# Optimization experiments

Hardware: AMD Instinct MI355X
Metric: run time of the kernel (lower is better)

## Reference

```python
import math
import jax, jax.numpy as jnp
import numpy as np

D = 1024
H = 16
DK = D // H
B = 4
L = 2048


def setup_inputs() -> dict:
    key = jax.random.key(0)
    ks = jax.random.split(key, 11)
    s = 1.0 / math.sqrt(D)
    return {
        "q": jax.random.normal(ks[0], (B, L, D), jnp.float32),
        "k": jax.random.normal(ks[1], (B, L, D), jnp.float32),
        "v": jax.random.normal(ks[2], (B, L, D), jnp.float32),
        "wq_w": jax.random.normal(ks[3], (D, D), jnp.float32) * s,
        "wq_b": jnp.zeros((D,), jnp.float32),
        "wk_w": jax.random.normal(ks[4], (D, D), jnp.float32) * s,
        "wk_b": jnp.zeros((D,), jnp.float32),
        "wv_w": jax.random.normal(ks[5], (D, D), jnp.float32) * s,
        "wv_b": jnp.zeros((D,), jnp.float32),
        "wo_w": jax.random.normal(ks[6], (D, D), jnp.float32) * s,
        "wo_b": jnp.zeros((D,), jnp.float32),
    }


def reference(q, k, v, wq_w, wq_b, wk_w, wk_b, wv_w, wv_b, wo_w, wo_b):
    # torch Linear: x @ W.T + b
    Q = (q @ wq_w.T + wq_b).reshape(B, L, H, DK).transpose(0, 2, 1, 3)  # [B,H,L,DK]
    K = (k @ wk_w.T + wk_b).reshape(B, -1, H, DK).transpose(0, 2, 1, 3)
    V = (v @ wv_w.T + wv_b).reshape(B, -1, H, DK).transpose(0, 2, 1, 3)
    sc = jnp.einsum("bhqd,bhkd->bhqk", Q, K) / math.sqrt(DK)  # [B,H,L,L]
    # causal mask: strictly upper triangular filled with -1e9
    cm = jnp.triu(jnp.ones((L, L), dtype=bool), 1)
    sc = jnp.where(cm, jnp.float32(-1e9), sc)
    at = jax.nn.softmax(sc, axis=-1)  # dropout p=0 (eval)
    out = jnp.einsum("bhqk,bhkd->bhqd", at, V)  # [B,H,L,DK]
    out = out.transpose(0, 2, 1, 3).reshape(B, L, D)
    return out @ wo_w.T + wo_b
```

## Files before the change

### kernel.cpp

```cpp
#include <hip/hip_runtime.h>
#include <stdint.h>

#define DD 1024
#define NH 16
#define DHEAD 64
#define NB 4
#define SEQ 2048
#define MR (NB*SEQ)
#define NT (SEQ/128)

typedef __attribute__((ext_vector_type(8))) short s8v;
typedef __attribute__((ext_vector_type(4))) float f4v;

__device__ __forceinline__ unsigned short f2bf(float f) {
  union { float f; uint32_t u; } c; c.f = f;
  uint32_t u = c.u;
  u += 0x7fffu + ((u >> 16) & 1u);
  return (unsigned short)(u >> 16);
}
__device__ __forceinline__ unsigned short f2bf_trunc(float f) {
  union { float f; uint32_t u; } c; c.f = f;
  return (unsigned short)(c.u >> 16);
}

__device__ __forceinline__ void load_lds16(const void* g, void* lds) {
  __builtin_amdgcn_global_load_lds(
      (__attribute__((address_space(1))) void*)(uintptr_t)g,
      (__attribute__((address_space(3))) void*)(uint32_t)(uintptr_t)lds,
      16, 0, 0);
}

__global__ void cvt_all(
    const float* __restrict__ q, const float* __restrict__ k, const float* __restrict__ v,
    const float* __restrict__ w0, const float* __restrict__ w1,
    const float* __restrict__ w2, const float* __restrict__ w3,
    unsigned short* __restrict__ qb, unsigned short* __restrict__ kb,
    unsigned short* __restrict__ vb,
    unsigned short* __restrict__ w0b, unsigned short* __restrict__ w1b,
    unsigned short* __restrict__ w2b, unsigned short* __restrict__ w3b)
{
  int blk = blockIdx.x;
  const float* src; unsigned short* dst; size_t off;
  if (blk < 12288) {
    int a = blk >> 12;
    src = a == 0 ? q : (a == 1 ? k : v);
    dst = a == 0 ? qb : (a == 1 ? kb : vb);
    off = (size_t)(blk & 4095) * 2048;
  } else {
    int wb = blk - 12288;
    int a = wb >> 9;
    src = a == 0 ? w0 : (a == 1 ? w1 : (a == 2 ? w2 : w3));
    dst = a == 0 ? w0b : (a == 1 ? w1b : (a == 2 ? w2b : w3b));
    off = (size_t)(wb & 511) * 2048;
  }
  size_t i = off + (size_t)threadIdx.x * 8;
  float4 a4 = *(const float4*)(src + i);
  float4 b4 = *(const float4*)(src + i + 4);
  union { unsigned short us[8]; uint4 u; } t;
  t.us[0] = f2bf(a4.x); t.us[1] = f2bf(a4.y); t.us[2] = f2bf(a4.z); t.us[3] = f2bf(a4.w);
  t.us[4] = f2bf(b4.x); t.us[5] = f2bf(b4.y); t.us[6] = f2bf(b4.z); t.us[7] = f2bf(b4.w);
  *(uint4*)(dst + i) = t.u;
}

__global__ __launch_bounds__(256, 2) void gemm_bt(
    const unsigned short* __restrict__ A,
    const unsigned short* __restrict__ Bw,
    const float* __restrict__ bias,
    float* __restrict__ Cout)
{
  __shared__ __align__(16) short As[64 * 64];
  __shared__ __align__(16) short Bs[128 * 64];
  const int linear = blockIdx.y * 8 + blockIdx.x;
  const int nx = linear >> 7;
  const int my = linear & 127;
  const int tid = threadIdx.x;
  const int wave = tid >> 6, lane = tid & 63;
  const int wm = (wave >> 1) * 32, wn = (wave & 1) * 64;
  const int lr = lane & 15, lg = lane >> 4;
  const unsigned short* Ab = A + (size_t)my * 64 * DD;
  const unsigned short* Bb = Bw + (size_t)nx * 128 * DD;

  f4v z = {0.f, 0.f, 0.f, 0.f};
  f4v acc[2][4];
  for (int mi = 0; mi < 2; mi++) for (int ni = 0; ni < 4; ni++) acc[mi][ni] = z;

  for (int k0 = 0; k0 < DD; k0 += 64) {
    __syncthreads();
    for (int i = 0; i < 2; i++) {
      int c = tid + i * 256;
      int row = c >> 3, kc = (c & 7) << 3;
      load_lds16(Ab + (size_t)row * DD + k0 + kc, As + c * 8);
    }
    for (int i = 0; i < 4; i++) {
      int c = tid + i * 256;
      int row = c >> 3, kc = (c & 7) << 3;
      load_lds16(Bb + (size_t)row * DD + k0 + kc, Bs + c * 8);
    }
    __syncthreads();
    for (int kk = 0; kk < 64; kk += 32) {
      s8v af[2], bf[4];
      for (int i = 0; i < 2; i++)
        af[i] = *(const s8v*)(As + (wm + i * 16 + lr) * 64 + kk + lg * 8);
      for (int i = 0; i < 4; i++)
        bf[i] = *(const s8v*)(Bs + (wn + i * 16 + lr) * 64 + kk + lg * 8);
      for (int mi = 0; mi < 2; mi++)
        for (int ni = 0; ni < 4; ni++)
          acc[mi][ni] = __builtin_amdgcn_mfma_f32_16x16x32_bf16(af[mi], bf[ni], acc[mi][ni], 0, 0, 0);
    }
  }
  for (int ni = 0; ni < 4; ni++) {
    int col = nx * 128 + wn + ni * 16 + lr;
    float bv = bias[col];
    for (int mi = 0; mi < 2; mi++) {
      int row0 = my * 64 + wm + mi * 16 + lg * 4;
      for (int r = 0; r < 4; r++)
        Cout[(size_t)(row0 + r) * DD + col] = acc[mi][ni][r] + bv;
    }
  }
}

__global__ __launch_bounds__(256, 2) void gemm_qkv(
    const unsigned short* __restrict__ qA, const unsigned short* __restrict__ kA,
    const unsigned short* __restrict__ vA,
    const unsigned short* __restrict__ wq, const unsigned short* __restrict__ wk,
    const unsigned short* __restrict__ wv,
    const float* __restrict__ bq, const float* __restrict__ bk, const float* __restrict__ bv,
    unsigned short* __restrict__ Qp, unsigned short* __restrict__ Kp,
    unsigned short* __restrict__ VpT)
{
  __shared__ __align__(16) short As[128 * 64];
  __shared__ __align__(16) short Bs[128 * 64];
  const int linear = blockIdx.y * 24 + blockIdx.x;
  const int nx  = linear / 192;
  const int rem = linear % 192;
  const int seg = rem >> 6;
  const int my  = rem & 63;
  const unsigned short* A  = seg == 0 ? qA : (seg == 1 ? kA : vA);
  const unsigned short* Bw = seg == 0 ? wq : (seg == 1 ? wk : wv);
  const float* bias        = seg == 0 ? bq : (seg == 1 ? bk : bv);

  const int tid = threadIdx.x;
  const int wave = tid >> 6, lane = tid & 63;
  const int wm = (wave >> 1) * 64, wn = (wave & 1) * 64;
  const int lr = lane & 15, lg = lane >> 4;
  const unsigned short* Ab = A + (size_t)my * 128 * DD;
  const unsigned short* Bb = Bw + (size_t)nx * 128 * DD;

  f4v z = {0.f, 0.f, 0.f, 0.f};
  f4v acc[4][4];
  for (int mi = 0; mi < 4; mi++) for (int ni = 0; ni < 4; ni++) acc[mi][ni] = z;

  for (int k0 = 0; k0 < DD; k0 += 64) {
    __syncthreads();
    for (int i = 0; i < 4; i++) {
      int c = tid + i * 256;
      int row = c >> 3, kc = (c & 7) << 3;
      load_lds16(Ab + (size_t)row * DD + k0 + kc, As + c * 8);
      load_lds16(Bb + (size_t)row * DD + k0 + kc, Bs + c * 8);
    }
    __syncthreads();
    for (int kk = 0; kk < 64; kk += 32) {
      s8v af[4], bf[4];
      for (int i = 0; i < 4; i++)
        af[i] = *(const s8v*)(As + (wm + i * 16 + lr) * 64 + kk + lg * 8);
      for (int i = 0; i < 4; i++)
        bf[i] = *(const s8v*)(Bs + (wn + i * 16 + lr) * 64 + kk + lg * 8);
      for (int mi = 0; mi < 4; mi++)
        for (int ni = 0; ni < 4; ni++)
          acc[mi][ni] = __builtin_amdgcn_mfma_f32_16x16x32_bf16(af[mi], bf[ni], acc[mi][ni], 0, 0, 0);
    }
  }
  if (seg < 2) {
    unsigned short* Cout = seg == 0 ? Qp : Kp;
    for (int ni = 0; ni < 4; ni++) {
      int col = nx * 128 + wn + ni * 16 + lr;
      float bv = bias[col];
      for (int mi = 0; mi < 4; mi++) {
        int row0 = my * 128 + wm + mi * 16 + lg * 4;
        for (int r = 0; r < 4; r++)
          Cout[(size_t)(row0 + r) * DD + col] = f2bf(acc[mi][ni][r] + bv);
      }
    }
  } else {
    for (int ni = 0; ni < 4; ni++) {
      int col = nx * 128 + wn + ni * 16 + lr;
      float bv = bias[col];
      int hh = col >> 6, dd = col & 63;
      for (int mi = 0; mi < 4; mi++) {
        int row0 = my * 128 + wm + mi * 16 + lg * 4;
        int bb = row0 >> 11, ll = row0 & 2047;
        uint64_t w = 0;
        for (int r = 0; r < 4; r++)
          w |= (uint64_t)f2bf(acc[mi][ni][r] + bv) << (16 * r);
        *(uint64_t*)(VpT + ((size_t)(bb * NH + hh) * 64 + dd) * SEQ + ll) = w;
      }
    }
  }
}

#define KS_STRIDE 72
#define VT_STRIDE 136
#define PS_STRIDE 72

__device__ __forceinline__ void attn_step(
    const s8v (&qf)[2][2], const s8v (&kf)[2][4],
    f4v (&o)[2][4], float (&ls)[2][4],
    int qbase, int colbase,
    const short* __restrict__ Vt, int vsub, short* __restrict__ Pw,
    int lr, int lg)
{
  const float csc = 0.125f * 1.44269504089f;
  const float FM = 14.0f;
  f4v zv = {0.f, 0.f, 0.f, 0.f};
  f4v s[2][4];
  for (int mi = 0; mi < 2; mi++) for (int ni = 0; ni < 4; ni++) s[mi][ni] = zv;
  for (int ks = 0; ks < 2; ks++)
    for (int mi = 0; mi < 2; mi++)
      for (int ni = 0; ni < 4; ni++)
        s[mi][ni] = __builtin_amdgcn_mfma_f32_16x16x32_bf16(qf[mi][ks], kf[ks][ni], s[mi][ni], 0, 0, 0);
  const bool diag = (colbase + 63 > qbase);
  for (int mi = 0; mi < 2; mi++)
    for (int ni = 0; ni < 4; ni++)
      for (int r = 0; r < 4; r++) {
        float e = __builtin_amdgcn_exp2f(fmaf(s[mi][ni][r], csc, -FM));
        if (diag) {
          int row = qbase + mi * 16 + lg * 4 + r;
          int col = colbase + ni * 16 + lr;
          e = (col > row) ? 0.f : e;
        }
        ls[mi][r] += e;
        Pw[(mi * 16 + lg * 4 + r) * PS_STRIDE + ni * 16 + lr] = (short)f2bf_trunc(e);
      }
  for (int kc2 = 0; kc2 < 2; kc2++) {
    s8v pf[2], vf[4];
    for (int mi = 0; mi < 2; mi++)
      pf[mi] = *(const s8v*)(Pw + (mi * 16 + lr) * PS_STRIDE + kc2 * 32 + lg * 8);
    for (int ni = 0; ni < 4; ni++)
      vf[ni] = *(const s8v*)(Vt + (ni * 16 + lr) * VT_STRIDE + vsub + kc2 * 32 + lg * 8);
    for (int mi = 0; mi < 2; mi++)
      for (int ni = 0; ni < 4; ni++)
        o[mi][ni] = __builtin_amdgcn_mfma_f32_16x16x32_bf16(pf[mi], vf[ni], o[mi][ni], 0, 0, 0);
  }
}

__global__ __launch_bounds__(256, 2) void fattn(
    const unsigned short* __restrict__ Qp,
    const unsigned short* __restrict__ Kp,
    const unsigned short* __restrict__ VpT,
    unsigned short* __restrict__ Op)
{
  __shared__ __align__(16) short Ks[128 * KS_STRIDE];
  __shared__ __align__(16) short Vt[64 * VT_STRIDE];
  __shared__ __align__(16) short Ps[4 * 32 * PS_STRIDE];
  const int tid = threadIdx.x;
  const int wave = tid >> 6, lane = tid & 63;
  const int lr = lane & 15, lg = lane >> 4;
  const int linear = blockIdx.y * 8 + blockIdx.x;
  const int xA = linear >> 6;
  const int bh = linear & 63;
  const int b = bh >> 4, h = bh & 15;
  const int xB = NT - 1 - xA;
  const int qbA = xA * 128 + wave * 32;
  const int qbB = xB * 128 + wave * 32;
  const unsigned short* Qrow = Qp + ((size_t)b * SEQ) * DD + h * DHEAD;
  const unsigned short* Krow = Kp + ((size_t)b * SEQ) * DD + h * DHEAD;
  const unsigned short* VT   = VpT + (size_t)bh * 64 * SEQ;
  short* Pw = Ps + wave * (32 * PS_STRIDE);

  s8v qfA[2][2], qfB[2][2];
  for (int mi = 0; mi < 2; mi++)
    for (int ks = 0; ks < 2; ks++) {
      qfA[mi][ks] = *(const s8v*)(Qrow + (size_t)(qbA + mi * 16 + lr) * DD + ks * 32 + lg * 8);
      qfB[mi][ks] = *(const s8v*)(Qrow + (size_t)(qbB + mi * 16 + lr) * DD + ks * 32 + lg * 8);
    }

  f4v zv = {0.f, 0.f, 0.f, 0.f};
  f4v oA[2][4], oB[2][4];
  float lA[2][4], lB[2][4];
  for (int mi = 0; mi < 2; mi++)
    for (int r = 0; r < 4; r++) { lA[mi][r] = 0.f; lB[mi][r] = 0.f; }
  for (int mi = 0; mi < 2; mi++)
    for (int ni = 0; ni < 4; ni++) { oA[mi][ni] = zv; oB[mi][ni] = zv; }

  const int npair = xB + 1;

  for (int p = 0; p < npair; p++) {
    s8v kreg[4], vreg[4];
    int krow[4], kkc[4], vd[4], vkc[4];
    for (int i = 0; i < 4; i++) {
      int c = tid + i * 256;
      krow[i] = c >> 3; kkc[i] = (c & 7) << 3;
      kreg[i] = *(const s8v*)(Krow + (size_t)(p * 128 + krow[i]) * DD + kkc[i]);
      vd[i] = c >> 4; vkc[i] = (c & 15) << 3;
      vreg[i] = *(const s8v*)(VT + (size_t)vd[i] * SEQ + p * 128 + vkc[i]);
    }
    __syncthreads();
    for (int i = 0; i < 4; i++) {
      *(s8v*)(Ks + krow[i] * KS_STRIDE + kkc[i]) = kreg[i];
      *(s8v*)(Vt + vd[i] * VT_STRIDE + vkc[i]) = vreg[i];
    }
    __syncthreads();
    for (int sub = 0; sub < 2; sub++) {
      int colbase = (2 * p + sub) * 64;
      bool actB = colbase <= qbB + 31;
      bool actA = colbase <= qbA + 31;
      if (actB || actA) {
        const short* KsSub = Ks + sub * 64 * KS_STRIDE;
        s8v kf[2][4];
        for (int ks = 0; ks < 2; ks++)
          for (int ni = 0; ni < 4; ni++)
            kf[ks][ni] = *(const s8v*)(KsSub + (ni * 16 + lr) * KS_STRIDE + ks * 32 + lg * 8);
        int vsub = sub * 64;
        if (actB) attn_step(qfB, kf, oB, lB, qbB, colbase, Vt, vsub, Pw, lr, lg);
        if (actA) attn_step(qfA, kf, oA, lA, qbA, colbase, Vt, vsub, Pw, lr, lg);
      }
    }
  }

  unsigned short* Orow = Op + ((size_t)b * SEQ) * DD + h * DHEAD;
  for (int mi = 0; mi < 2; mi++)
    for (int r = 0; r < 4; r++) {
      float sA = lA[mi][r], sB = lB[mi][r];
      for (int d2 = 1; d2 < 16; d2 <<= 1) {
        sA += __shfl_xor(sA, d2);
        sB += __shfl_xor(sB, d2);
      }
      float invA = 1.f / sA, invB = 1.f / sB;
      size_t rowA = (size_t)qbA + mi * 16 + lg * 4 + r;
      size_t rowB = (size_t)qbB + mi * 16 + lg * 4 + r;
      for (int ni = 0; ni < 4; ni++) {
        Orow[rowA * DD + ni * 16 + lr] = f2bf(oA[mi][ni][r] * invA);
        Orow[rowB * DD + ni * 16 + lr] = f2bf(oB[mi][ni][r] * invB);
      }
    }
}

extern "C" void kernel_launch(void* const* d_in, const int* in_sizes, int n_in,
                              void* d_out, int out_size, void* d_ws, size_t ws_size,
                              hipStream_t stream) {
  const float* q    = (const float*)d_in[0];
  const float* k    = (const float*)d_in[1];
  const float* v    = (const float*)d_in[2];
  const float* wq_w = (const float*)d_in[3];
  const float* wq_b = (const float*)d_in[4];
  const float* wk_w = (const float*)d_in[5];
  const float* wk_b = (const float*)d_in[6];
  const float* wv_w = (const float*)d_in[7];
  const float* wv_b = (const float*)d_in[8];
  const float* wo_w = (const float*)d_in[9];
  const float* wo_b = (const float*)d_in[10];

  const size_t BIG = (size_t)MR * DD;
  const size_t WSZ = (size_t)DD * DD;
  unsigned short* p = (unsigned short*)d_ws;
  unsigned short* qb  = p; p += BIG;
  unsigned short* kb  = p; p += BIG;
  unsigned short* vb  = p; p += BIG;
  unsigned short* wqb = p; p += WSZ;
  unsigned short* wkb = p; p += WSZ;
  unsigned short* wvb = p; p += WSZ;
  unsigned short* wob = p; p += WSZ;
  unsigned short* Qp  = p; p += BIG;
  unsigned short* Kp  = p; p += BIG;
  unsigned short* VpT = p; p += BIG;
  unsigned short* AO  = p; p += BIG;

  cvt_all<<<dim3(14336), dim3(256), 0, stream>>>(
      q, k, v, wq_w, wk_w, wv_w, wo_w, qb, kb, vb, wqb, wkb, wvb, wob);

  gemm_qkv<<<dim3(24, MR / 128), dim3(256), 0, stream>>>(
      qb, kb, vb, wqb, wkb, wvb, wq_b, wk_b, wv_b, Qp, Kp, VpT);

  fattn<<<dim3(NT / 2, NB * NH), dim3(256), 0, stream>>>(Qp, Kp, VpT, AO);

  gemm_bt<<<dim3(8, 128), dim3(256), 0, stream>>>(AO, wob, wo_b, (float*)d_out);

  (void)in_sizes; (void)n_in; (void)out_size; (void)ws_size;
}
```

Baseline: 326.9 us.

## Fuse fp32-to-bf16 activation conversion into QKV GEMM and swizzle LDS tiles

Removes the separate conversion pass over q/k/v. The QKV GEMM now loads fp32 activations directly into registers, converts them to bf16, and stores them to LDS, prefetching the next k-slice into registers while the MFMAs run. An XOR swizzle on LDS columns is added to both GEMMs to reduce bank conflicts on the fragment reads. This trades roughly 150MB of bf16 write and read traffic for twice the fp32 global reads inside the GEMM, each A tile being re-read by 8 column blocks. It also adds register pressure from the prefetch buffers.

```diff
diff --git a/kernel.cpp b/kernel.cpp
--- a/kernel.cpp
+++ b/kernel.cpp
@@ -30,30 +30,24 @@
       16, 0, 0);
 }
 
-__global__ void cvt_all(
-    const float* __restrict__ q, const float* __restrict__ k, const float* __restrict__ v,
+__device__ __forceinline__ s8v pack8(float4 a, float4 b) {
+  union { unsigned short us[8]; s8v v; } t;
+  t.us[0] = f2bf(a.x); t.us[1] = f2bf(a.y); t.us[2] = f2bf(a.z); t.us[3] = f2bf(a.w);
+  t.us[4] = f2bf(b.x); t.us[5] = f2bf(b.y); t.us[6] = f2bf(b.z); t.us[7] = f2bf(b.w);
+  return t.v;
+}
+
+__global__ void cvt_w(
     const float* __restrict__ w0, const float* __restrict__ w1,
     const float* __restrict__ w2, const float* __restrict__ w3,
-    unsigned short* __restrict__ qb, unsigned short* __restrict__ kb,
-    unsigned short* __restrict__ vb,
-    unsigned short* __restrict__ w0b, unsigned short* __restrict__ w1b,
-    unsigned short* __restrict__ w2b, unsigned short* __restrict__ w3b)
+    unsigned short* __restrict__ d0, unsigned short* __restrict__ d1,
+    unsigned short* __restrict__ d2, unsigned short* __restrict__ d3)
 {
   int blk = blockIdx.x;
-  const float* src; unsigned short* dst; size_t off;
-  if (blk < 12288) {
-    int a = blk >> 12;
-    src = a == 0 ? q : (a == 1 ? k : v);
-    dst = a == 0 ? qb : (a == 1 ? kb : vb);
-    off = (size_t)(blk & 4095) * 2048;
-  } else {
-    int wb = blk - 12288;
-    int a = wb >> 9;
-    src = a == 0 ? w0 : (a == 1 ? w1 : (a == 2 ? w2 : w3));
-    dst = a == 0 ? w0b : (a == 1 ? w1b : (a == 2 ? w2b : w3b));
-    off = (size_t)(wb & 511) * 2048;
-  }
-  size_t i = off + (size_t)threadIdx.x * 8;
+  int a = blk >> 9;
+  const float* src = a == 0 ? w0 : (a == 1 ? w1 : (a == 2 ? w2 : w3));
+  unsigned short* dst = a == 0 ? d0 : (a == 1 ? d1 : (a == 2 ? d2 : d3));
+  size_t i = (size_t)(blk & 511) * 2048 + (size_t)threadIdx.x * 8;
   float4 a4 = *(const float4*)(src + i);
   float4 b4 = *(const float4*)(src + i + 4);
   union { unsigned short us[8]; uint4 u; } t;
@@ -77,6 +71,7 @@
   const int wave = tid >> 6, lane = tid & 63;
   const int wm = (wave >> 1) * 32, wn = (wave & 1) * 64;
   const int lr = lane & 15, lg = lane >> 4;
+  const int sw = lr & 7;
   const unsigned short* Ab = A + (size_t)my * 64 * DD;
   const unsigned short* Bb = Bw + (size_t)nx * 128 * DD;
 
@@ -88,21 +83,22 @@
     __syncthreads();
     for (int i = 0; i < 2; i++) {
       int c = tid + i * 256;
-      int row = c >> 3, kc = (c & 7) << 3;
-      load_lds16(Ab + (size_t)row * DD + k0 + kc, As + c * 8);
+      int row = c >> 3, pg = c & 7;
+      load_lds16(Ab + (size_t)row * DD + k0 + ((pg ^ (row & 7)) << 3), As + c * 8);
     }
     for (int i = 0; i < 4; i++) {
       int c = tid + i * 256;
-      int row = c >> 3, kc = (c & 7) << 3;
-      load_lds16(Bb + (size_t)row * DD + k0 + kc, Bs + c * 8);
+      int row = c >> 3, pg = c & 7;
+      load_lds16(Bb + (size_t)row * DD + k0 + ((pg ^ (row & 7)) << 3), Bs + c * 8);
     }
     __syncthreads();
     for (int kk = 0; kk < 64; kk += 32) {
+      int gb = kk >> 3;
       s8v af[2], bf[4];
       for (int i = 0; i < 2; i++)
-        af[i] = *(const s8v*)(As + (wm + i * 16 + lr) * 64 + kk + lg * 8);
+        af[i] = *(const s8v*)(As + (wm + i * 16 + lr) * 64 + (((gb + lg) ^ sw) << 3));
       for (int i = 0; i < 4; i++)
-        bf[i] = *(const s8v*)(Bs + (wn + i * 16 + lr) * 64 + kk + lg * 8);
+        bf[i] = *(const s8v*)(Bs + (wn + i * 16 + lr) * 64 + (((gb + lg) ^ sw) << 3));
       for (int mi = 0; mi < 2; mi++)
         for (int ni = 0; ni < 4; ni++)
           acc[mi][ni] = __builtin_amdgcn_mfma_f32_16x16x32_bf16(af[mi], bf[ni], acc[mi][ni], 0, 0, 0);
@@ -120,8 +116,8 @@
 }
 
 __global__ __launch_bounds__(256, 2) void gemm_qkv(
-    const unsigned short* __restrict__ qA, const unsigned short* __restrict__ kA,
-    const unsigned short* __restrict__ vA,
+    const float* __restrict__ qA, const float* __restrict__ kA,
+    const float* __restrict__ vA,
     const unsigned short* __restrict__ wq, const unsigned short* __restrict__ wk,
     const unsigned short* __restrict__ wv,
     const float* __restrict__ bq, const float* __restrict__ bk, const float* __restrict__ bv,
@@ -135,7 +131,7 @@
   const int rem = linear % 192;
   const int seg = rem >> 6;
   const int my  = rem & 63;
-  const unsigned short* A  = seg == 0 ? qA : (seg == 1 ? kA : vA);
+  const float* A          = seg == 0 ? qA : (seg == 1 ? kA : vA);
   const unsigned short* Bw = seg == 0 ? wq : (seg == 1 ? wk : wv);
   const float* bias        = seg == 0 ? bq : (seg == 1 ? bk : bv);
 
@@ -143,8 +139,20 @@
   const int wave = tid >> 6, lane = tid & 63;
   const int wm = (wave >> 1) * 64, wn = (wave & 1) * 64;
   const int lr = lane & 15, lg = lane >> 4;
-  const unsigned short* Ab = A + (size_t)my * 128 * DD;
+  const int sw = lr & 7;
+  const float* Ab = A + (size_t)my * 128 * DD;
   const unsigned short* Bb = Bw + (size_t)nx * 128 * DD;
+
+  int arow[4], ag[4];
+  s8v areg[4];
+  for (int i = 0; i < 4; i++) {
+    int c = tid + i * 256;
+    arow[i] = c >> 3; ag[i] = c & 7;
+  }
+  for (int i = 0; i < 4; i++) {
+    const float* src = Ab + (size_t)arow[i] * DD + (ag[i] << 3);
+    areg[i] = pack8(*(const float4*)src, *(const float4*)(src + 4));
+  }
 
   f4v z = {0.f, 0.f, 0.f, 0.f};
   f4v acc[4][4];
@@ -152,19 +160,27 @@
 
   for (int k0 = 0; k0 < DD; k0 += 64) {
     __syncthreads();
+    for (int i = 0; i < 4; i++)
+      *(s8v*)(As + arow[i] * 64 + ((ag[i] ^ (arow[i] & 7)) << 3)) = areg[i];
     for (int i = 0; i < 4; i++) {
       int c = tid + i * 256;
-      int row = c >> 3, kc = (c & 7) << 3;
-      load_lds16(Ab + (size_t)row * DD + k0 + kc, As + c * 8);
-      load_lds16(Bb + (size_t)row * DD + k0 + kc, Bs + c * 8);
-    }
-    __syncthreads();
+      int row = c >> 3, pg = c & 7;
+      load_lds16(Bb + (size_t)row * DD + k0 + ((pg ^ (row & 7)) << 3), Bs + c * 8);
+    }
+    __syncthreads();
+    if (k0 + 64 < DD) {
+      for (int i = 0; i < 4; i++) {
+        const float* src = Ab + (size_t)arow[i] * DD + k0 + 64 + (ag[i] << 3);
+        areg[i] = pack8(*(const float4*)src, *(const float4*)(src + 4));
+      }
+    }
     for (int kk = 0; kk < 64; kk += 32) {
+      int gb = kk >> 3;
       s8v af[4], bf[4];
       for (int i = 0; i < 4; i++)
-        af[i] = *(const s8v*)(As + (wm + i * 16 + lr) * 64 + kk + lg * 8);
+        af[i] = *(const s8v*)(As + (wm + i * 16 + lr) * 64 + (((gb + lg) ^ sw) << 3));
       for (int i = 0; i < 4; i++)
-        bf[i] = *(const s8v*)(Bs + (wn + i * 16 + lr) * 64 + kk + lg * 8);
+        bf[i] = *(const s8v*)(Bs + (wn + i * 16 + lr) * 64 + (((gb + lg) ^ sw) << 3));
       for (int mi = 0; mi < 4; mi++)
         for (int ni = 0; ni < 4; ni++)
           acc[mi][ni] = __builtin_amdgcn_mfma_f32_16x16x32_bf16(af[mi], bf[ni], acc[mi][ni], 0, 0, 0);
@@ -353,9 +369,6 @@
   const size_t BIG = (size_t)MR * DD;
   const size_t WSZ = (size_t)DD * DD;
   unsigned short* p = (unsigned short*)d_ws;
-  unsigned short* qb  = p; p += BIG;
-  unsigned short* kb  = p; p += BIG;
-  unsigned short* vb  = p; p += BIG;
   unsigned short* wqb = p; p += WSZ;
   unsigned short* wkb = p; p += WSZ;
   unsigned short* wvb = p; p += WSZ;
@@ -365,11 +378,11 @@
   unsigned short* VpT = p; p += BIG;
   unsigned short* AO  = p; p += BIG;
 
-  cvt_all<<<dim3(14336), dim3(256), 0, stream>>>(
-      q, k, v, wq_w, wk_w, wv_w, wo_w, qb, kb, vb, wqb, wkb, wvb, wob);
+  cvt_w<<<dim3(2048), dim3(256), 0, stream>>>(
+      wq_w, wk_w, wv_w, wo_w, wqb, wkb, wvb, wob);
 
   gemm_qkv<<<dim3(24, MR / 128), dim3(256), 0, stream>>>(
-      qb, kb, vb, wqb, wkb, wvb, wq_b, wk_b, wv_b, Qp, Kp, VpT);
+      q, k, v, wqb, wkb, wvb, wq_b, wk_b, wv_b, Qp, Kp, VpT);
 
   fattn<<<dim3(NT / 2, NB * NH), dim3(256), 0, stream>>>(Qp, Kp, VpT, AO);
 
```

Result: no change. 325.4 us (-0.5%).
